# Kernel tuning notes

Hardware: AMD Instinct MI355X
Metric: run time of the kernel (lower is better)

## Reference

```python
import jax, jax.numpy as jnp
import numpy as np

CHUNK = 64

def depthwise_fir(x, filt):
    # x: [B,N,H,D]; filt: [H,D,K]; causal depthwise FIR conv along N
    B, N, H, D = x.shape
    K = filt.shape[-1]
    xc = x.reshape(B, N, H * D).transpose(0, 2, 1)  # [B, HD, N]
    xc = jnp.pad(xc, ((0, 0), (0, 0), (K - 1, 0)))
    w = filt.reshape(H * D, 1, K)
    y = jax.lax.conv_general_dilated(xc, w, (1,), 'VALID',
                                     feature_group_count=H * D,
                                     dimension_numbers=('NCH', 'OIH', 'NCH'))
    return y.transpose(0, 2, 1).reshape(B, N, H, D)

def delta_rule_chunkwise(q, k, v, beta, chunk=CHUNK):
    # DeltaNet chunkwise parallel delta rule. q,k,v:[B,H,L,D], beta:[B,H,L]
    B, H, L, D = q.shape
    q = q * (D ** -0.5)
    k = k / (jnp.linalg.norm(k, axis=-1, keepdims=True) + 1e-6)  # l2-norm keys (DeltaNet convention)
    v = v * beta[..., None]
    k_beta = k * beta[..., None]
    n = L // chunk
    toc = lambda t: t.reshape(B, H, n, chunk, D)
    qc, kc, vc, kbc = toc(q), toc(k), toc(v), toc(k_beta)
    # T = (I + strict_lower(k_beta k^T))^{-1} via triangular solve
    A = jnp.tril(jnp.einsum('bhncd,bhnmd->bhncm', kbc, kc), -1)
    I = jnp.eye(chunk, dtype=q.dtype)
    T = jax.scipy.linalg.solve_triangular(I + A, jnp.broadcast_to(I, A.shape), lower=True)
    u = T @ vc   # [B,H,n,c,D]
    w = T @ kbc  # [B,H,n,c,D]
    def step(S, inp):
        q_i, k_i, u_i, w_i = inp                 # [B,H,c,D]
        u_t = u_i - w_i @ S
        attn_i = jnp.tril(jnp.einsum('bhcd,bhmd->bhcm', q_i, k_i))
        o_i = q_i @ S + attn_i @ u_t
        S = S + jnp.einsum('bhcd,bhce->bhde', k_i, u_t)
        return S, o_i
    xs = tuple(jnp.moveaxis(t, 2, 0) for t in (qc, kc, u, w))
    S0 = jnp.zeros((B, H, D, D), dtype=q.dtype)
    S, o = jax.lax.scan(step, S0, xs)
    o = jnp.moveaxis(o, 0, 2).reshape(B, H, L, D)
    return o, S

def setup_inputs() -> dict:
    key = jax.random.key(0)
    B, N, C, H = 4, 1024, 768, 12
    D = C // H
    P = 5
    ks = jax.random.split(key, 16)
    s = 0.02
    fir_s = jnp.zeros((H, D, 3)).at[..., -1].set(1.0) + 0.01 * jax.random.normal(ks[1], (H, D, 3))
    fir_l = jnp.zeros((H, D, 7)).at[..., -1].set(1.0) + 0.01 * jax.random.normal(ks[2], (H, D, 7))
    return {
        'x': jax.random.normal(ks[0], (B, N, C), jnp.float32),
        'w_qkv': s * jax.random.normal(ks[3], (C, 3 * C)),
        'w_proj': s * jax.random.normal(ks[4], (C, C)),
        'b_proj': jnp.zeros((C,)),
        'fir_short_w': fir_s,
        'fir_long_w': fir_l,
        'mix': 0.02 * jax.random.normal(ks[5], (H, H)),
        'w_prune': s * jax.random.normal(ks[6], (C, H * P)),
        'b_prune': jnp.zeros((H * P,)),
        'w_g1': s * jax.random.normal(ks[7], (C, C)),
        'b_g1': jnp.zeros((C,)),
        'w_g2': s * jax.random.normal(ks[8], (C, H)),
        'b_g2': jnp.zeros((H,)),
        'w_id': s * jax.random.normal(ks[9], (C, C)),
        'id_static_logit': jnp.full((H,), float(np.log(0.2 / 0.8)), jnp.float32),
        'w_idgate': s * jax.random.normal(ks[10], (C, H)),
        'b_idgate': jnp.full((H,), -1.5, jnp.float32),
    }

def reference(x, w_qkv, w_proj, b_proj, fir_short_w, fir_long_w, mix, w_prune,
              b_prune, w_g1, b_g1, w_g2, b_g2, w_id, id_static_logit, w_idgate, b_idgate):
    B, N, C = x.shape
    H = id_static_logit.shape[0]
    D = C // H
    qkv = (x @ w_qkv).reshape(B, N, 3, H, D).transpose(2, 0, 3, 1, 4)  # [3,B,H,N,D]
    q, k, v = qkv[0], qkv[1], qkv[2]
    scale = D ** -0.5
    scores = jnp.einsum('bhqd,bhkd->bhqk', q, k) * scale
    # causal softmax attention (fp8 sage-attention math in full precision)
    neg = jnp.finfo(scores.dtype).min
    causal = jnp.tril(jnp.ones((N, N), dtype=bool))
    attn = jax.nn.softmax(jnp.where(causal, scores, neg), axis=-1)
    attn_out = jnp.einsum('bhqk,bhkd->bnhd'.replace('n', 'q'), attn, v).transpose(0, 2, 1, 3)  # [B,N,H,D] (unused downstream, kept for fidelity)
    v_reshaped = v.transpose(0, 2, 1, 3)  # [B,N,H,D]
    # identity path with static*dynamic gate
    identity_out = (x @ w_id).reshape(B, N, H, D)
    dyn_gate = jax.nn.sigmoid(x @ w_idgate + b_idgate)   # [B,N,H]
    static_gate = jax.nn.sigmoid(id_static_logit)
    identity_out = identity_out * (dyn_gate * static_gate)[..., None]
    # beta = row-sums of (non-causal) softmax, per source (== ~1 numerically)
    beta = jax.nn.softmax(scores, axis=-1).sum(-1)       # [B,H,N]
    delta_out = delta_rule_chunkwise(q, k, v, beta)[0].transpose(0, 2, 1, 3)  # [B,N,H,D]
    # FIR paths + cross-head mixing (residual head-mixing matrix)
    fir_s = depthwise_fir(v_reshaped, fir_short_w)
    fir_l = depthwise_fir(v_reshaped, fir_long_w)
    mix_s = fir_s + jnp.einsum('bnhd,hg->bngd', fir_s, mix)
    mix_l = fir_l + jnp.einsum('bnhd,hg->bngd', fir_l, mix)
    paths = jnp.stack([mix_s, mix_l, delta_out, v_reshaped, identity_out], 0)  # [P,B,N,H,D]
    P = paths.shape[0]
    # progressive pruning: per-head softmax over paths + entropy loss
    wts = jax.nn.softmax((x @ w_prune + b_prune).reshape(B, N, H, P), axis=-1)
    pruned = jnp.einsum('pbnhd,bnhp->bnhd', paths, wts)
    ent1 = -jnp.mean(jnp.sum(wts * jnp.log(wts + 1e-8), -1))
    # context gating: MLP -> per-head sigmoid gate + binary entropy loss
    hdn = jax.nn.gelu(x @ w_g1 + b_g1)
    gate = jax.nn.sigmoid(hdn @ w_g2 + b_g2)             # [B,N,H]
    context = pruned * gate[..., None]
    ent2 = -jnp.mean(gate * jnp.log(gate + 1e-8) + (1 - gate) * jnp.log(1 - gate + 1e-8))
    out = context.reshape(B, N, C) @ w_proj + b_proj
    return out, ent1 + ent2
```

## Files before the change

kernel.cpp:

```cpp
#include <hip/hip_runtime.h>
#include <hip/hip_bf16.h>
#include <math.h>

#define Bz 4
#define Nn 1024
#define Cc 768
#define Hh 12
#define Dd 64
#define BN 4096
#define NC 16
#define BH 48
#define OUT_ELEMS 3145728

#define WS_QKV     0u
#define WS_WSP     9437184u
#define WS_GL      16252928u
#define WS_QS      16777216u
#define WS_KNT     19922944u
#define WS_U       23068672u
#define WS_DELTA   32505856u
#define WS_ENT     38797312u
#define WS_FIRST   38798336u
#define WS_FIRLT   38800640u
#define WS_CBIAS   38806016u
#define WS_GBIAS   38807680u
#define WS_BF16    38807808u
#define SH_XB      0u
#define SH_WQKVT   3145728u
#define SH_WCATT   4915200u
#define SH_G2T     6193152u
#define SH_WPROJT  6291456u
#define SH_HDNB    6881280u
#define SH_CTXB    10027008u

typedef __attribute__((ext_vector_type(8))) short bf16x8;
typedef __attribute__((ext_vector_type(4))) float f32x4;

__device__ __forceinline__ float sigmoidf_(float x) { return 1.f / (1.f + __expf(-x)); }
__device__ __forceinline__ float geluf_(float x) {
    float t = tanhf(0.7978845608028654f * (x + 0.044715f * x * x * x));
    return 0.5f * x * (1.f + t);
}
__device__ __forceinline__ short bf16c(float f) {
    union { float f; unsigned u; } a; a.f = f;
    unsigned r = a.u + 0x7fffu + ((a.u >> 16) & 1u);
    return (short)(r >> 16);
}
__device__ __forceinline__ void gload16(const void* g, void* l) {
    __builtin_amdgcn_global_load_lds(
        (const __attribute__((address_space(1))) unsigned*)g,
        (__attribute__((address_space(3))) unsigned*)l, 16, 0, 0);
}
__device__ __forceinline__ bf16x8 frag_(const short* arr, int row, int kc, int quad) {
    return *(const bf16x8*)&arr[row * 64 + (((kc * 4 + quad) ^ (row & 7)) << 3)];
}

__global__ __launch_bounds__(256) void convert_x_kernel(const float* __restrict__ src,
        short* __restrict__ dst, int n4) {
    int i = blockIdx.x * 256 + threadIdx.x;
    if (i < n4) {
        float4 v = *(const float4*)&src[(size_t)i * 4];
        short4 o;
        o.x = bf16c(v.x); o.y = bf16c(v.y); o.z = bf16c(v.z); o.w = bf16c(v.w);
        *(short4*)&dst[(size_t)i * 4] = o;
    }
}

__global__ __launch_bounds__(256) void convert_w_kernel(const float* __restrict__ w_qkv,
        const float* __restrict__ w_id, const float* __restrict__ w_g1,
        const float* __restrict__ w_proj, short* __restrict__ wqkvT,
        short* __restrict__ wcatT, short* __restrict__ wprojT,
        const float* __restrict__ wp, const float* __restrict__ wig,
        const float* __restrict__ bp, const float* __restrict__ big,
        const float* __restrict__ bg1, const float* __restrict__ bg2,
        const float* __restrict__ wg2, const float* __restrict__ firs,
        const float* __restrict__ firl, short* __restrict__ g2T,
        float* __restrict__ cbias, float* __restrict__ gbias,
        float* __restrict__ firsT, float* __restrict__ firlT) {
    __shared__ float t[64][65];
    const int z = blockIdx.z;
    const int tid = threadIdx.x;
    if (z == 4) {
        int i = (blockIdx.y * 12 + blockIdx.x) * 256 + tid;
        if (i < 98304) {
            int r = i / 768, k = i % 768;
            float wv = 0.f;
            if (r < 60) wv = wp[k * 60 + r];
            else if (r < 72) wv = wig[k * 12 + (r - 60)];
            wcatT[(size_t)(1536 + r) * 768 + k] = (r < 72) ? bf16c(wv) : (short)0;
            g2T[(size_t)r * 768 + k] = (r < 12) ? bf16c(wg2[k * 12 + r]) : (short)0;
        }
        if (i < 1664) {
            float bv = 0.f;
            if (i >= 768 && i < 1536) bv = bg1[i - 768];
            else if (i >= 1536 && i < 1596) bv = bp[i - 1536];
            else if (i >= 1596 && i < 1608) bv = big[i - 1596];
            cbias[i] = bv;
        }
        if (i < 128) gbias[i] = (i < 12) ? bg2[i] : 0.f;
        if (i < 2304) { int tt = i / 768, e = i % 768; firsT[tt * 768 + e] = firs[e * 3 + tt]; }
        if (i < 5376) { int tt = i / 768, e = i % 768; firlT[tt * 768 + e] = firl[e * 7 + tt]; }
        return;
    }
    const float* src; short* dst; int Nw;
    if (z == 0)      { src = w_qkv;  dst = wqkvT;              Nw = 2304; }
    else if (z == 1) { src = w_id;   dst = wcatT;              Nw = 768; }
    else if (z == 2) { src = w_g1;   dst = wcatT + 768 * 768;  Nw = 768; }
    else             { src = w_proj; dst = wprojT;             Nw = 768; }
    const int n0 = blockIdx.y * 64;
    if (n0 >= Nw) return;
    const int k0 = blockIdx.x * 64;
    for (int e = tid; e < 1024; e += 256) {
        int r = e >> 4, c4 = (e & 15) * 4;
        float4 v = *(const float4*)&src[(size_t)(k0 + r) * Nw + n0 + c4];
        t[c4 + 0][r] = v.x; t[c4 + 1][r] = v.y;
        t[c4 + 2][r] = v.z; t[c4 + 3][r] = v.w;
    }
    __syncthreads();
    for (int e = tid; e < 1024; e += 256) {
        int r = e >> 4, c4 = (e & 15) * 4;
        short4 o;
        o.x = bf16c(t[r][c4 + 0]); o.y = bf16c(t[r][c4 + 1]);
        o.z = bf16c(t[r][c4 + 2]); o.w = bf16c(t[r][c4 + 3]);
        *(short4*)&dst[(size_t)(n0 + r) * 768 + k0 + c4] = o;
    }
}

__global__ __launch_bounds__(256) void gemm_mfma(const short* __restrict__ A,
        const short* __restrict__ BT, const float* __restrict__ bias,
        float* __restrict__ C, int M, int N, int K, int glo, int ghi,
        short* __restrict__ C2) {
    __shared__ short As[128 * 64];
    __shared__ short Bs[128 * 64];
    const int tid = threadIdx.x;
    const int lane = tid & 63, w = tid >> 6;
    const int quad = lane >> 4, l15 = lane & 15;
    const int row0 = blockIdx.y * 128, col0 = blockIdx.x * 128;
    const int wm = (w >> 1) * 64, wn = (w & 1) * 64;

    int srow[4]; int scol[4];
#pragma unroll
    for (int i = 0; i < 4; ++i) {
        int G = (w * 4 + i) * 64 + lane;
        int row = G >> 3, g = G & 7;
        srow[i] = row;
        scol[i] = (g ^ (row & 7)) * 8;
    }
    int aoff[4][2], boff[4][2];
#pragma unroll
    for (int mi = 0; mi < 4; ++mi)
#pragma unroll
        for (int kk = 0; kk < 2; ++kk) {
            int ra = wm + mi * 16 + l15;
            aoff[mi][kk] = ra * 128 + (((kk * 4 + quad) ^ (ra & 7)) * 16);
            int rb = wn + mi * 16 + l15;
            boff[mi][kk] = rb * 128 + (((kk * 4 + quad) ^ (rb & 7)) * 16);
        }

    f32x4 acc[4][4];
#pragma unroll
    for (int mi = 0; mi < 4; ++mi)
#pragma unroll
        for (int ni = 0; ni < 4; ++ni) acc[mi][ni] = (f32x4)0.f;

    for (int k0 = 0; k0 < K; k0 += 64) {
#pragma unroll
        for (int i = 0; i < 4; ++i) {
            gload16(&A[(size_t)(row0 + srow[i]) * K + k0 + scol[i]], &As[(w * 4 + i) * 512]);
            gload16(&BT[(size_t)(col0 + srow[i]) * K + k0 + scol[i]], &Bs[(w * 4 + i) * 512]);
        }
        __syncthreads();
#pragma unroll
        for (int kk = 0; kk < 2; ++kk) {
            bf16x8 af[4], bfr[4];
#pragma unroll
            for (int mi = 0; mi < 4; ++mi)
                af[mi] = *(const bf16x8*)((const char*)As + aoff[mi][kk]);
#pragma unroll
            for (int ni = 0; ni < 4; ++ni)
                bfr[ni] = *(const bf16x8*)((const char*)Bs + boff[ni][kk]);
#pragma unroll
            for (int mi = 0; mi < 4; ++mi)
#pragma unroll
                for (int ni = 0; ni < 4; ++ni)
                    acc[mi][ni] = __builtin_amdgcn_mfma_f32_16x16x32_bf16(
                        af[mi], bfr[ni], acc[mi][ni], 0, 0, 0);
        }
        __syncthreads();
    }
#pragma unroll
    for (int ni = 0; ni < 4; ++ni) {
        int col = col0 + wn + ni * 16 + l15;
        float bv = bias ? bias[col] : 0.f;
        bool gel = (col >= glo) && (col < ghi);
#pragma unroll
        for (int mi = 0; mi < 4; ++mi) {
#pragma unroll
            for (int r = 0; r < 4; ++r) {
                int row = row0 + wm + mi * 16 + quad * 4 + r;
                float v = acc[mi][ni][r] + bv;
                if (gel) v = geluf_(v);
                C[(size_t)row * N + col] = v;
                if (C2 && gel) C2[(size_t)row * 768 + (col - glo)] = bf16c(v);
            }
        }
    }
}

__global__ __launch_bounds__(256) void pre_kernel(const float* __restrict__ qkv,
        short* __restrict__ Qsb16, short* __restrict__ Kntb16, float* __restrict__ U,
        short* __restrict__ Wb16, short* __restrict__ Atb16) {
    __shared__ __align__(16) char smem[50176];
    float (*ts)[68] = (float (*)[68])smem;
    short* kn  = (short*)(smem + 17408);
    short* knt = (short*)(smem + 25600);
    short* qsb = (short*)(smem + 33792);
    short* vtb = (short*)(smem + 41984);
    float (*zbuf)[68] = (float (*)[68])(smem + 17408);
    short* tb  = (short*)(smem + 33792);
    const int blk = blockIdx.x;
    const int c = blk & 15, bh = blk >> 4;
    const int b = bh / Hh, h = bh % Hh;
    const int tid = threadIdx.x;
    const int lane = tid & 63, w = tid >> 6;
    const int quad = lane >> 4, l15 = lane & 15;
    const int r = tid >> 2, d0 = (tid & 3) * 16;
    const size_t rowbase = ((size_t)(b * Nn + c * 64)) * (3 * Cc) + h * 64;
    const size_t base2 = (size_t)blk * 4096;

    {
        float4 qq[4], kq[4], vq[4];
        const float* bp_ = &qkv[rowbase + (size_t)r * 2304 + d0];
#pragma unroll
        for (int t4 = 0; t4 < 4; ++t4) qq[t4] = *(const float4*)&bp_[t4 * 4];
#pragma unroll
        for (int t4 = 0; t4 < 4; ++t4) kq[t4] = *(const float4*)&bp_[768 + t4 * 4];
#pragma unroll
        for (int t4 = 0; t4 < 4; ++t4) vq[t4] = *(const float4*)&bp_[1536 + t4 * 4];

        float kf[16];
#pragma unroll
        for (int t4 = 0; t4 < 4; ++t4) {
            kf[t4 * 4 + 0] = kq[t4].x; kf[t4 * 4 + 1] = kq[t4].y;
            kf[t4 * 4 + 2] = kq[t4].z; kf[t4 * 4 + 3] = kq[t4].w;
        }
        float ss = 0.f;
#pragma unroll
        for (int t = 0; t < 16; ++t) ss += kf[t] * kf[t];
        ss += __shfl_xor(ss, 1);
        ss += __shfl_xor(ss, 2);
        float invn = 1.f / (sqrtf(ss) + 1e-6f);
#pragma unroll
        for (int t = 0; t < 16; ++t) kf[t] *= invn;
        {
            bf16x8 g0, g1;
#pragma unroll
            for (int t = 0; t < 8; ++t) { g0[t] = bf16c(kf[t]); g1[t] = bf16c(kf[8 + t]); }
            int gb = d0 >> 3;
            *(bf16x8*)&kn[r * 64 + (((gb + 0) ^ (r & 7)) << 3)] = g0;
            *(bf16x8*)&kn[r * 64 + (((gb + 1) ^ (r & 7)) << 3)] = g1;
#pragma unroll
            for (int t = 0; t < 16; ++t) {
                int d = d0 + t;
                knt[d * 64 + (((r >> 3) ^ (d & 7)) << 3) + (r & 7)] = bf16c(kf[t]);
            }
        }
        {
            float qf[16];
#pragma unroll
            for (int t4 = 0; t4 < 4; ++t4) {
                qf[t4 * 4 + 0] = qq[t4].x * 0.125f; qf[t4 * 4 + 1] = qq[t4].y * 0.125f;
                qf[t4 * 4 + 2] = qq[t4].z * 0.125f; qf[t4 * 4 + 3] = qq[t4].w * 0.125f;
            }
            bf16x8 g0, g1;
#pragma unroll
            for (int t = 0; t < 8; ++t) { g0[t] = bf16c(qf[t]); g1[t] = bf16c(qf[8 + t]); }
            int gb = d0 >> 3;
            *(bf16x8*)&qsb[r * 64 + (((gb + 0) ^ (r & 7)) << 3)] = g0;
            *(bf16x8*)&qsb[r * 64 + (((gb + 1) ^ (r & 7)) << 3)] = g1;
            *(bf16x8*)&Qsb16[base2 + r * 64 + d0] = g0;
            *(bf16x8*)&Qsb16[base2 + r * 64 + d0 + 8] = g1;
        }
#pragma unroll
        for (int t4 = 0; t4 < 4; ++t4) {
            int d = d0 + t4 * 4;
            vtb[(d + 0) * 64 + (((r >> 3) ^ ((d + 0) & 7)) << 3) + (r & 7)] = bf16c(vq[t4].x);
            vtb[(d + 1) * 64 + (((r >> 3) ^ ((d + 1) & 7)) << 3) + (r & 7)] = bf16c(vq[t4].y);
            vtb[(d + 2) * 64 + (((r >> 3) ^ ((d + 2) & 7)) << 3) + (r & 7)] = bf16c(vq[t4].z);
            vtb[(d + 3) * 64 + (((r >> 3) ^ ((d + 3) & 7)) << 3) + (r & 7)] = bf16c(vq[t4].w);
        }
    }
    __syncthreads();

    f32x4 accT[4];
    {
        const int ar = w * 16 + l15;
        bf16x8 aK0 = frag_(kn, ar, 0, quad), aK1 = frag_(kn, ar, 1, quad);
        bf16x8 aQ0 = frag_(qsb, ar, 0, quad), aQ1 = frag_(qsb, ar, 1, quad);
        f32x4 accA[4];
#pragma unroll
        for (int ni = 0; ni < 4; ++ni) {
            int br = ni * 16 + l15;
            bf16x8 b0 = frag_(kn, br, 0, quad), b1 = frag_(kn, br, 1, quad);
            accA[ni] = __builtin_amdgcn_mfma_f32_16x16x32_bf16(aK0, b0, (f32x4)0.f, 0, 0, 0);
            accA[ni] = __builtin_amdgcn_mfma_f32_16x16x32_bf16(aK1, b1, accA[ni], 0, 0, 0);
            accT[ni] = __builtin_amdgcn_mfma_f32_16x16x32_bf16(aQ0, b0, (f32x4)0.f, 0, 0, 0);
            accT[ni] = __builtin_amdgcn_mfma_f32_16x16x32_bf16(aQ1, b1, accT[ni], 0, 0, 0);
        }
#pragma unroll
        for (int ni = 0; ni < 4; ++ni)
#pragma unroll
            for (int reg = 0; reg < 4; ++reg) {
                int row = w * 16 + quad * 4 + reg;
                int col = ni * 16 + l15;
                ts[row][col] = (col < row) ? accA[ni][reg] : 0.f;
            }
    }
    __syncthreads();

    {
        const int R0 = w * 16;
        const int j = lane & 15, s = lane >> 4;
#pragma unroll 1
        for (int i = 0; i < 16; ++i) {
            float p = 0.f;
            for (int m = s; m < i; m += 4)
                p += ts[R0 + i][R0 + m] * ts[R0 + m][R0 + j];
            p += __shfl_xor(p, 16);
            p += __shfl_xor(p, 32);
            if (s == 0) ts[R0 + i][R0 + j] = ((j == i) ? 1.f : 0.f) - p;
        }
    }
    __syncthreads();
#pragma unroll 1
    for (int I = 1; I < 4; ++I) {
        const int ncol = I * 16;
        for (int e = tid; e < 16 * ncol; e += 256) {
            int i = e / ncol, jj = e % ncol;
            float s = 0.f;
            for (int m = jj; m < ncol; ++m) s += ts[ncol + i][m] * ts[m][jj];
            zbuf[i][jj] = s;
        }
        __syncthreads();
        for (int e = tid; e < 16 * ncol; e += 256) {
            int i = e / ncol, jj = e % ncol;
            float s = 0.f;
            for (int ml = 0; ml <= i; ++ml) s += ts[ncol + i][ncol + ml] * zbuf[ml][jj];
            ts[ncol + i][jj] = -s;
        }
        __syncthreads();
    }
    for (int e = tid; e < 512; e += 256) {
        int row = e >> 3, g = e & 7;
        bf16x8 o;
#pragma unroll
        for (int t = 0; t < 8; ++t) o[t] = bf16c(ts[row][g * 8 + t]);
        *(bf16x8*)&tb[row * 64 + ((g ^ (row & 7)) << 3)] = o;
    }
    __syncthreads();

    f32x4 accW[4], accU[4];
    {
        const int ar = w * 16 + l15;
        bf16x8 aT0 = frag_(tb, ar, 0, quad), aT1 = frag_(tb, ar, 1, quad);
#pragma unroll
        for (int ni = 0; ni < 4; ++ni) {
            int br = ni * 16 + l15;
            bf16x8 b0 = frag_(knt, br, 0, quad), b1 = frag_(knt, br, 1, quad);
            bf16x8 c0 = frag_(vtb, br, 0, quad), c1 = frag_(vtb, br, 1, quad);
            accW[ni] = __builtin_amdgcn_mfma_f32_16x16x32_bf16(aT0, b0, (f32x4)0.f, 0, 0, 0);
            accW[ni] = __builtin_amdgcn_mfma_f32_16x16x32_bf16(aT1, b1, accW[ni], 0, 0, 0);
            accU[ni] = __builtin_amdgcn_mfma_f32_16x16x32_bf16(aT0, c0, (f32x4)0.f, 0, 0, 0);
            accU[ni] = __builtin_amdgcn_mfma_f32_16x16x32_bf16(aT1, c1, accU[ni], 0, 0, 0);
        }
    }
#pragma unroll
    for (int ni = 0; ni < 4; ++ni)
#pragma unroll
        for (int reg = 0; reg < 4; ++reg) {
            int row = w * 16 + quad * 4 + reg;
            int col = ni * 16 + l15;
            Wb16[base2 + (size_t)row * 64 + col] = bf16c(accW[ni][reg]);
            U[base2 + (size_t)row * 64 + col] = accU[ni][reg];
            Atb16[base2 + (size_t)row * 64 + col] =
                (col <= row) ? bf16c(accT[ni][reg]) : (short)0;
        }
    for (int e = tid; e < 512; e += 256) {
        int row = e >> 3, gl = e & 7;
        *(bf16x8*)&Kntb16[base2 + row * 64 + ((gl ^ (row & 7)) << 3)] =
            *(const bf16x8*)&knt[row * 64 + (gl << 3)];
    }
}

#define LOADF(cc, F, UU) {                                                     \
    size_t tb_ = ((size_t)(bh * 16 + (cc))) * 4096;                            \
    F##0 = *(const bf16x8*)&Wb16[tb_ + off0];                                  \
    F##1 = *(const bf16x8*)&Wb16[tb_ + off1];                                  \
    F##2 = *(const bf16x8*)&Qsb16[tb_ + off0];                                 \
    F##3 = *(const bf16x8*)&Qsb16[tb_ + off1];                                 \
    F##4 = *(const bf16x8*)&Atb16[tb_ + off0];                                 \
    F##5 = *(const bf16x8*)&Atb16[tb_ + off1];                                 \
    F##6 = *(const bf16x8*)&Kntb16[tb_ + off0];                                \
    F##7 = *(const bf16x8*)&Kntb16[tb_ + off1];                                \
    UU##0 = U[tb_ + urow + 0 * 64]; UU##1 = U[tb_ + urow + 1 * 64];            \
    UU##2 = U[tb_ + urow + 2 * 64]; UU##3 = U[tb_ + urow + 3 * 64]; }

#define BODY(c, F, UU, FN, UN) {                                               \
    int cn_ = ((c) + 1 < 16) ? (c) + 1 : 0;                                    \
    LOADF(cn_, FN, UN);                                                        \
    bf16x8 st0 = *(const bf16x8*)&ST[stoff0];                                  \
    bf16x8 st1 = *(const bf16x8*)&ST[stoff1];                                  \
    bf16x8 nw0, nw1;                                                           \
    _Pragma("unroll") for (int t_ = 0; t_ < 8; ++t_) {                         \
        nw0[t_] = F##0[t_] ^ (short)0x8000;                                    \
        nw1[t_] = F##1[t_] ^ (short)0x8000; }                                  \
    f32x4 ut = {UU##0, UU##1, UU##2, UU##3};                                   \
    ut = __builtin_amdgcn_mfma_f32_16x16x32_bf16(nw0, st0, ut, 0, 0, 0);       \
    ut = __builtin_amdgcn_mfma_f32_16x16x32_bf16(nw1, st1, ut, 0, 0, 0);       \
    f32x4 o = (f32x4)0.f;                                                      \
    o = __builtin_amdgcn_mfma_f32_16x16x32_bf16(F##2, st0, o, 0, 0, 0);        \
    o = __builtin_amdgcn_mfma_f32_16x16x32_bf16(F##3, st1, o, 0, 0, 0);        \
    _Pragma("unroll") for (int j_ = 0; j_ < 4; ++j_) {                         \
        int rr_ = R0 + quad * 4 + j_;                                          \
        UT[l15 * 64 + (((rr_ >> 3) ^ (l15 & 7)) << 3) + (rr_ & 7)] = bf16c(ut[j_]); } \
    __syncthreads();                                                           \
    bf16x8 uf0 = *(const bf16x8*)&UT[stoff0];                                  \
    bf16x8 uf1 = *(const bf16x8*)&UT[stoff1];                                  \
    o = __builtin_amdgcn_mfma_f32_16x16x32_bf16(F##4, uf0, o, 0, 0, 0);        \
    o = __builtin_amdgcn_mfma_f32_16x16x32_bf16(F##5, uf1, o, 0, 0, 0);        \
    S = __builtin_amdgcn_mfma_f32_16x16x32_bf16(F##6, uf0, S, 0, 0, 0);        \
    S = __builtin_amdgcn_mfma_f32_16x16x32_bf16(F##7, uf1, S, 0, 0, 0);        \
    _Pragma("unroll") for (int j_ = 0; j_ < 4; ++j_)                           \
        delta[obase + (size_t)((c) * 64 + j_) * 768] = o[j_];                  \
    _Pragma("unroll") for (int j_ = 0; j_ < 4; ++j_) {                         \
        int dd_ = R0 + quad * 4 + j_;                                          \
        ST[l15 * 64 + (((dd_ >> 3) ^ (l15 & 7)) << 3) + (dd_ & 7)] = bf16c(S[j_]); } \
    __syncthreads(); }

__global__ __launch_bounds__(256) void scan_kernel(const short* __restrict__ Qsb16,
        const short* __restrict__ Kntb16, const float* __restrict__ U,
        const short* __restrict__ Wb16, const short* __restrict__ Atb16,
        float* __restrict__ delta) {
    __shared__ short ST[1024];
    __shared__ short UT[1024];
    const int bh = blockIdx.x;
    const int b = bh / Hh, h = bh % Hh;
    const int g0 = blockIdx.y * 16;
    const int tid = threadIdx.x;
    const int lane = tid & 63, w = tid >> 6;
    const int quad = lane >> 4, l15 = lane & 15;
    const int R0 = w * 16;
    const int off0 = (R0 + l15) * 64 + quad * 8;
    const int off1 = off0 + 32;
    const int urow = (R0 + quad * 4) * 64 + g0 + l15;
    const int stoff0 = l15 * 64 + ((quad ^ (l15 & 7)) << 3);
    const int stoff1 = l15 * 64 + (((4 + quad) ^ (l15 & 7)) << 3);
    const size_t obase = ((size_t)(b * Nn + R0 + quad * 4)) * 768 + h * 64 + g0 + l15;

    for (int e = tid; e < 512; e += 256) ((int*)ST)[e] = 0;
    f32x4 S = (f32x4)0.f;
    bf16x8 fA0, fA1, fA2, fA3, fA4, fA5, fA6, fA7;
    bf16x8 fB0, fB1, fB2, fB3, fB4, fB5, fB6, fB7;
    float uA0, uA1, uA2, uA3, uB0, uB1, uB2, uB3;
    LOADF(0, fA, uA);
    __syncthreads();
#pragma unroll 1
    for (int c = 0; c < 16; c += 2) {
        BODY(c, fA, uA, fB, uB);
        BODY(c + 1, fB, uB, fA, uA);
    }
}

__global__ __launch_bounds__(256) void paths_kernel(const float* __restrict__ qkv,
        const float* __restrict__ delta, const float* __restrict__ wsp,
        const float* __restrict__ gl, const float* __restrict__ mixw,
        const float* __restrict__ idst, const float* __restrict__ firsT,
        const float* __restrict__ firlT, short* __restrict__ ctxb,
        float* __restrict__ entslots) {
    __shared__ float vt[10][768];
    __shared__ float fsb[768], flb[768];
    __shared__ float wts4[4][60], gate4[4][12], idg4[4][12];
    __shared__ float entb[48];
    const int blk = blockIdx.x;
    const int b = blk >> 8, n0 = (blk & 255) * 4;
    const int tid = threadIdx.x;

    for (int t = tid; t < 1920; t += 256) {
        int row = t / 192, c4 = (t % 192) * 4;
        int np = n0 - 6 + row;
        float4 v = make_float4(0.f, 0.f, 0.f, 0.f);
        if (np >= 0) v = *(const float4*)&qkv[((size_t)((b << 10) + np)) * 2304 + 1536 + c4];
        *(float4*)&vt[row][c4] = v;
    }
    if (tid < 48) {
        int ni = tid / 12, h = tid % 12;
        int bn = (b << 10) + n0 + ni;
        const float* pb = &wsp[(size_t)bn * 1664 + 1536];
        float lg[5]; float mx = -1e30f;
#pragma unroll
        for (int p = 0; p < 5; ++p) { lg[p] = pb[h * 5 + p]; mx = fmaxf(mx, lg[p]); }
        float sum = 0.f;
#pragma unroll
        for (int p = 0; p < 5; ++p) { lg[p] = __expf(lg[p] - mx); sum += lg[p]; }
        float e1 = 0.f;
#pragma unroll
        for (int p = 0; p < 5; ++p) {
            float wv = lg[p] / sum;
            wts4[ni][h * 5 + p] = wv;
            e1 += wv * logf(wv + 1e-8f);
        }
        float g = sigmoidf_(gl[(size_t)bn * 128 + h]);
        gate4[ni][h] = g;
        float e2 = g * logf(g + 1e-8f) + (1.f - g) * logf(1.f - g + 1e-8f);
        idg4[ni][h] = sigmoidf_(pb[60 + h]) * sigmoidf_(idst[h]);
        entb[tid] = e1 + e2;
    }
    float4 wl[7], wsv[3];
    if (tid < 192) {
        int c4 = tid * 4;
#pragma unroll
        for (int t = 0; t < 7; ++t) wl[t] = *(const float4*)&firlT[t * 768 + c4];
#pragma unroll
        for (int t = 0; t < 3; ++t) wsv[t] = *(const float4*)&firsT[t * 768 + c4];
    }
    __syncthreads();

#pragma unroll 1
    for (int ni = 0; ni < 4; ++ni) {
        if (tid < 192) {
            int c4 = tid * 4;
            float4 as = make_float4(0.f, 0.f, 0.f, 0.f);
            float4 al = make_float4(0.f, 0.f, 0.f, 0.f);
#pragma unroll
            for (int t = 0; t < 7; ++t) {
                float4 vv = *(const float4*)&vt[ni + t][c4];
                al.x += wl[t].x * vv.x; al.y += wl[t].y * vv.y;
                al.z += wl[t].z * vv.z; al.w += wl[t].w * vv.w;
                if (t >= 4) {
                    as.x += wsv[t - 4].x * vv.x; as.y += wsv[t - 4].y * vv.y;
                    as.z += wsv[t - 4].z * vv.z; as.w += wsv[t - 4].w * vv.w;
                }
            }
            *(float4*)&fsb[c4] = as;
            *(float4*)&flb[c4] = al;
        }
        __syncthreads();
        if (tid < 192) {
            int c4 = tid * 4;
            int h = c4 >> 6, d = c4 & 63;
            float4 ms = *(const float4*)&fsb[c4];
            float4 ml = *(const float4*)&flb[c4];
#pragma unroll
            for (int hh = 0; hh < 12; ++hh) {
                float mw = mixw[hh * 12 + h];
                float4 fsv = *(const float4*)&fsb[hh * 64 + d];
                float4 flv = *(const float4*)&flb[hh * 64 + d];
                ms.x += mw * fsv.x; ms.y += mw * fsv.y;
                ms.z += mw * fsv.z; ms.w += mw * fsv.w;
                ml.x += mw * flv.x; ml.y += mw * flv.y;
                ml.z += mw * flv.z; ml.w += mw * flv.w;
            }
            int bn = (b << 10) + n0 + ni;
            float4 dl = *(const float4*)&delta[(size_t)bn * 768 + c4];
            float4 iv = *(const float4*)&wsp[(size_t)bn * 1664 + c4];
            float4 vv = *(const float4*)&vt[ni + 6][c4];
            float ig = idg4[ni][h];
            const float* wp = &wts4[ni][h * 5];
            float4 pr;
            pr.x = ms.x * wp[0] + ml.x * wp[1] + dl.x * wp[2] + vv.x * wp[3] + iv.x * ig * wp[4];
            pr.y = ms.y * wp[0] + ml.y * wp[1] + dl.y * wp[2] + vv.y * wp[3] + iv.y * ig * wp[4];
            pr.z = ms.z * wp[0] + ml.z * wp[1] + dl.z * wp[2] + vv.z * wp[3] + iv.z * ig * wp[4];
            pr.w = ms.w * wp[0] + ml.w * wp[1] + dl.w * wp[2] + vv.w * wp[3] + iv.w * ig * wp[4];
            float g = gate4[ni][h];
            short4 o;
            o.x = bf16c(pr.x * g); o.y = bf16c(pr.y * g);
            o.z = bf16c(pr.z * g); o.w = bf16c(pr.w * g);
            *(short4*)&ctxb[(size_t)bn * 768 + c4] = o;
        }
        __syncthreads();
    }
    if (tid == 0) {
        float s = 0.f;
#pragma unroll
        for (int i = 0; i < 48; ++i) s += entb[i];
        entslots[blk] = s;
    }
}

__global__ __launch_bounds__(256) void finalize_kernel(const float* __restrict__ slots,
        float* __restrict__ out) {
    __shared__ float red[256];
    const int tid = threadIdx.x;
    float s = 0.f;
    for (int i = tid; i < 1024; i += 256) s += slots[i];
    red[tid] = s;
    __syncthreads();
    for (int off = 128; off > 0; off >>= 1) {
        if (tid < off) red[tid] += red[tid + off];
        __syncthreads();
    }
    if (tid == 0) out[OUT_ELEMS] = -red[0] * (1.f / 49152.f);
}

extern "C" void kernel_launch(void* const* d_in, const int* in_sizes, int n_in,
                              void* d_out, int out_size, void* d_ws, size_t ws_size,
                              hipStream_t stream) {
    const float* x        = (const float*)d_in[0];
    const float* w_qkv    = (const float*)d_in[1];
    const float* w_proj   = (const float*)d_in[2];
    const float* b_proj   = (const float*)d_in[3];
    const float* fir_s_w  = (const float*)d_in[4];
    const float* fir_l_w  = (const float*)d_in[5];
    const float* mixw     = (const float*)d_in[6];
    const float* w_prune  = (const float*)d_in[7];
    const float* b_prune  = (const float*)d_in[8];
    const float* w_g1     = (const float*)d_in[9];
    const float* b_g1     = (const float*)d_in[10];
    const float* w_g2     = (const float*)d_in[11];
    const float* b_g2     = (const float*)d_in[12];
    const float* w_id     = (const float*)d_in[13];
    const float* id_st    = (const float*)d_in[14];
    const float* w_idgate = (const float*)d_in[15];
    const float* b_idgate = (const float*)d_in[16];
    float* out = (float*)d_out;
    float* ws  = (float*)d_ws;

    float* qkv   = ws + WS_QKV;
    float* wsp   = ws + WS_WSP;
    float* gl    = ws + WS_GL;
    short* Qsb16  = (short*)(ws + WS_QS);
    short* Kntb16 = Qsb16 + 3145728;
    short* Wb16   = (short*)(ws + WS_KNT);
    short* Atb16  = Wb16 + 3145728;
    float* Ub    = ws + WS_U;
    float* delta = ws + WS_DELTA;
    float* ent   = ws + WS_ENT;
    float* firsT = ws + WS_FIRST;
    float* firlT = ws + WS_FIRLT;
    float* cbias = ws + WS_CBIAS;
    float* gbias = ws + WS_GBIAS;
    short* wsh   = (short*)(ws + WS_BF16);
    short* xb     = wsh + SH_XB;
    short* wqkvT  = wsh + SH_WQKVT;
    short* wcatT  = wsh + SH_WCATT;
    short* g2T    = wsh + SH_G2T;
    short* wprojT = wsh + SH_WPROJT;
    short* hdnb   = wsh + SH_HDNB;
    short* ctxb   = wsh + SH_CTXB;

    convert_x_kernel<<<dim3(3072), 256, 0, stream>>>(x, xb, 786432);
    convert_w_kernel<<<dim3(12, 36, 5), 256, 0, stream>>>(w_qkv, w_id, w_g1, w_proj,
            wqkvT, wcatT, wprojT, w_prune, w_idgate, b_prune, b_idgate, b_g1, b_g2,
            w_g2, fir_s_w, fir_l_w, g2T, cbias, gbias, firsT, firlT);
    gemm_mfma<<<dim3(18, 32), 256, 0, stream>>>(xb, wqkvT, nullptr, qkv, BN, 2304, 768,
                                                0, 0, nullptr);
    gemm_mfma<<<dim3(13, 32), 256, 0, stream>>>(xb, wcatT, cbias, wsp, BN, 1664, 768,
                                                768, 1536, hdnb);
    gemm_mfma<<<dim3(1, 32), 256, 0, stream>>>(hdnb, g2T, gbias, gl, BN, 128, 768,
                                               0, 0, nullptr);
    pre_kernel<<<dim3(BH * NC), 256, 0, stream>>>(qkv, Qsb16, Kntb16, Ub, Wb16, Atb16);
    scan_kernel<<<dim3(BH, 4), 256, 0, stream>>>(Qsb16, Kntb16, Ub, Wb16, Atb16, delta);
    paths_kernel<<<dim3(1024), 256, 0, stream>>>(qkv, delta, wsp, gl, mixw, id_st,
                                                 firsT, firlT, ctxb, ent);
    gemm_mfma<<<dim3(6, 32), 256, 0, stream>>>(ctxb, wprojT, b_proj, out, BN, 768, 768,
                                               0, 0, nullptr);
    finalize_kernel<<<1, 256, 0, stream>>>(ent, out);
}
```

Measured before the change: 286.2 us.

## Merge QKV and side-projection GEMMs and store intermediates in bf16

The separate QKV GEMM and the identity/gate/prune GEMM become one wide GEMM over a concatenated weight matrix, which scatters its bf16 outputs to per-purpose buffers in the epilogue. The qkv, identity-output and delta intermediates move from fp32 to bf16, so downstream pre, scan and paths kernels read and write half the bytes. The intent is to cut a launch, reuse the A tile across all outputs and reduce memory traffic. In exchange, more intermediates are rounded to bf16, which adds precision loss, especially in the delta-rule inputs.

```diff
diff --git a/kernel.cpp b/kernel.cpp
--- a/kernel.cpp
+++ b/kernel.cpp
@@ -12,26 +12,28 @@
 #define BH 48
 #define OUT_ELEMS 3145728
 
-#define WS_QKV     0u
-#define WS_WSP     9437184u
-#define WS_GL      16252928u
-#define WS_QS      16777216u
-#define WS_KNT     19922944u
-#define WS_U       23068672u
-#define WS_DELTA   32505856u
-#define WS_ENT     38797312u
-#define WS_FIRST   38798336u
-#define WS_FIRLT   38800640u
-#define WS_CBIAS   38806016u
-#define WS_GBIAS   38807680u
-#define WS_BF16    38807808u
+#define WS_U       0u
+#define WS_PLIG    3145728u
+#define WS_GL      3670016u
+#define WS_ENT     4194304u
+#define WS_FIRST   4195328u
+#define WS_FIRLT   4197632u
+#define WS_CBIAS   4203008u
+#define WS_GBIAS   4206976u
+#define WS_SH      4207104u
 #define SH_XB      0u
-#define SH_WQKVT   3145728u
-#define SH_WCATT   4915200u
-#define SH_G2T     6193152u
-#define SH_WPROJT  6291456u
-#define SH_HDNB    6881280u
-#define SH_CTXB    10027008u
+#define SH_QKVB    3145728u
+#define SH_IDOUT   12582912u
+#define SH_HDNB    15728640u
+#define SH_CTXB    18874368u
+#define SH_DELTA   22020096u
+#define SH_QS      25165824u
+#define SH_KNT     28311552u
+#define SH_W       31457280u
+#define SH_AT      34603008u
+#define SH_WCAT2T  37748736u
+#define SH_G2T     40796160u
+#define SH_WPROJT  40894464u
 
 typedef __attribute__((ext_vector_type(8))) short bf16x8;
 typedef __attribute__((ext_vector_type(4))) float f32x4;
@@ -45,6 +47,11 @@
     union { float f; unsigned u; } a; a.f = f;
     unsigned r = a.u + 0x7fffu + ((a.u >> 16) & 1u);
     return (short)(r >> 16);
+}
+__device__ __forceinline__ float b2f(short s) {
+    union { float f; unsigned u; } a;
+    a.u = ((unsigned)(unsigned short)s) << 16;
+    return a.f;
 }
 __device__ __forceinline__ void gload16(const void* g, void* l) {
     __builtin_amdgcn_global_load_lds(
@@ -68,8 +75,8 @@
 
 __global__ __launch_bounds__(256) void convert_w_kernel(const float* __restrict__ w_qkv,
         const float* __restrict__ w_id, const float* __restrict__ w_g1,
-        const float* __restrict__ w_proj, short* __restrict__ wqkvT,
-        short* __restrict__ wcatT, short* __restrict__ wprojT,
+        const float* __restrict__ w_proj, short* __restrict__ wcat2T,
+        short* __restrict__ wprojT,
         const float* __restrict__ wp, const float* __restrict__ wig,
         const float* __restrict__ bp, const float* __restrict__ big,
         const float* __restrict__ bg1, const float* __restrict__ bg2,
@@ -87,14 +94,14 @@
             float wv = 0.f;
             if (r < 60) wv = wp[k * 60 + r];
             else if (r < 72) wv = wig[k * 12 + (r - 60)];
-            wcatT[(size_t)(1536 + r) * 768 + k] = (r < 72) ? bf16c(wv) : (short)0;
+            wcat2T[(size_t)(3840 + r) * 768 + k] = (r < 72) ? bf16c(wv) : (short)0;
             g2T[(size_t)r * 768 + k] = (r < 12) ? bf16c(wg2[k * 12 + r]) : (short)0;
         }
-        if (i < 1664) {
+        if (i < 3968) {
             float bv = 0.f;
-            if (i >= 768 && i < 1536) bv = bg1[i - 768];
-            else if (i >= 1536 && i < 1596) bv = bp[i - 1536];
-            else if (i >= 1596 && i < 1608) bv = big[i - 1596];
+            if (i >= 3072 && i < 3840) bv = bg1[i - 3072];
+            else if (i >= 3840 && i < 3900) bv = bp[i - 3840];
+            else if (i >= 3900 && i < 3912) bv = big[i - 3900];
             cbias[i] = bv;
         }
         if (i < 128) gbias[i] = (i < 12) ? bg2[i] : 0.f;
@@ -103,10 +110,10 @@
         return;
     }
     const float* src; short* dst; int Nw;
-    if (z == 0)      { src = w_qkv;  dst = wqkvT;              Nw = 2304; }
-    else if (z == 1) { src = w_id;   dst = wcatT;              Nw = 768; }
-    else if (z == 2) { src = w_g1;   dst = wcatT + 768 * 768;  Nw = 768; }
-    else             { src = w_proj; dst = wprojT;             Nw = 768; }
+    if (z == 0)      { src = w_qkv;  dst = wcat2T;               Nw = 2304; }
+    else if (z == 1) { src = w_id;   dst = wcat2T + 2304 * 768;  Nw = 768; }
+    else if (z == 2) { src = w_g1;   dst = wcat2T + 3072 * 768;  Nw = 768; }
+    else             { src = w_proj; dst = wprojT;               Nw = 768; }
     const int n0 = blockIdx.y * 64;
     if (n0 >= Nw) return;
     const int k0 = blockIdx.x * 64;
@@ -126,88 +133,103 @@
     }
 }
 
+#define GEMM_CORE(APTR, BPTR, KDIM)                                            \
+    __shared__ short As[128 * 64];                                             \
+    __shared__ short Bs[128 * 64];                                             \
+    const int tid = threadIdx.x;                                               \
+    const int lane = tid & 63, w = tid >> 6;                                   \
+    const int quad = lane >> 4, l15 = lane & 15;                               \
+    const int row0 = blockIdx.y * 128, col0 = blockIdx.x * 128;                \
+    const int wm = (w >> 1) * 64, wn = (w & 1) * 64;                           \
+    int srow[4]; int scol[4];                                                  \
+    _Pragma("unroll") for (int i = 0; i < 4; ++i) {                            \
+        int G = (w * 4 + i) * 64 + lane;                                       \
+        int row = G >> 3, g = G & 7;                                           \
+        srow[i] = row;                                                         \
+        scol[i] = (g ^ (row & 7)) * 8;                                         \
+    }                                                                          \
+    int aoff[4][2], boff[4][2];                                                \
+    _Pragma("unroll") for (int mi = 0; mi < 4; ++mi)                           \
+        _Pragma("unroll") for (int kk = 0; kk < 2; ++kk) {                     \
+            int ra = wm + mi * 16 + l15;                                       \
+            aoff[mi][kk] = ra * 128 + (((kk * 4 + quad) ^ (ra & 7)) * 16);     \
+            int rb = wn + mi * 16 + l15;                                       \
+            boff[mi][kk] = rb * 128 + (((kk * 4 + quad) ^ (rb & 7)) * 16);     \
+        }                                                                      \
+    f32x4 acc[4][4];                                                           \
+    _Pragma("unroll") for (int mi = 0; mi < 4; ++mi)                           \
+        _Pragma("unroll") for (int ni = 0; ni < 4; ++ni) acc[mi][ni] = (f32x4)0.f; \
+    for (int k0 = 0; k0 < (KDIM); k0 += 64) {                                  \
+        _Pragma("unroll") for (int i = 0; i < 4; ++i) {                        \
+            gload16(&(APTR)[(size_t)(row0 + srow[i]) * (KDIM) + k0 + scol[i]], \
+                    &As[(w * 4 + i) * 512]);                                   \
+            gload16(&(BPTR)[(size_t)(col0 + srow[i]) * (KDIM) + k0 + scol[i]], \
+                    &Bs[(w * 4 + i) * 512]);                                   \
+        }                                                                      \
+        __syncthreads();                                                       \
+        _Pragma("unroll") for (int kk = 0; kk < 2; ++kk) {                     \
+            bf16x8 af[4], bfr[4];                                              \
+            _Pragma("unroll") for (int mi = 0; mi < 4; ++mi)                   \
+                af[mi] = *(const bf16x8*)((const char*)As + aoff[mi][kk]);     \
+            _Pragma("unroll") for (int ni = 0; ni < 4; ++ni)                   \
+                bfr[ni] = *(const bf16x8*)((const char*)Bs + boff[ni][kk]);    \
+            _Pragma("unroll") for (int mi = 0; mi < 4; ++mi)                   \
+                _Pragma("unroll") for (int ni = 0; ni < 4; ++ni)               \
+                    acc[mi][ni] = __builtin_amdgcn_mfma_f32_16x16x32_bf16(     \
+                        af[mi], bfr[ni], acc[mi][ni], 0, 0, 0);                \
+        }                                                                      \
+        __syncthreads();                                                       \
+    }
+
+__global__ __launch_bounds__(256) void gemm_main(const short* __restrict__ A,
+        const short* __restrict__ BT, const float* __restrict__ bias,
+        short* __restrict__ qkvb, short* __restrict__ idoutb,
+        short* __restrict__ hdnb, float* __restrict__ plig) {
+    GEMM_CORE(A, BT, 768)
+#pragma unroll
+    for (int ni = 0; ni < 4; ++ni) {
+        int col = col0 + wn + ni * 16 + l15;
+        float bv = bias[col];
+#pragma unroll
+        for (int mi = 0; mi < 4; ++mi) {
+#pragma unroll
+            for (int r = 0; r < 4; ++r) {
+                int row = row0 + wm + mi * 16 + quad * 4 + r;
+                float v = acc[mi][ni][r] + bv;
+                if (col < 2304) {
+                    qkvb[(size_t)row * 2304 + col] = bf16c(v);
+                } else if (col < 3072) {
+                    idoutb[(size_t)row * 768 + (col - 2304)] = bf16c(v);
+                } else if (col < 3840) {
+                    hdnb[(size_t)row * 768 + (col - 3072)] = bf16c(geluf_(v));
+                } else {
+                    plig[(size_t)row * 128 + (col - 3840)] = v;
+                }
+            }
+        }
+    }
+}
+
 __global__ __launch_bounds__(256) void gemm_mfma(const short* __restrict__ A,
         const short* __restrict__ BT, const float* __restrict__ bias,
-        float* __restrict__ C, int M, int N, int K, int glo, int ghi,
-        short* __restrict__ C2) {
-    __shared__ short As[128 * 64];
-    __shared__ short Bs[128 * 64];
-    const int tid = threadIdx.x;
-    const int lane = tid & 63, w = tid >> 6;
-    const int quad = lane >> 4, l15 = lane & 15;
-    const int row0 = blockIdx.y * 128, col0 = blockIdx.x * 128;
-    const int wm = (w >> 1) * 64, wn = (w & 1) * 64;
-
-    int srow[4]; int scol[4];
-#pragma unroll
-    for (int i = 0; i < 4; ++i) {
-        int G = (w * 4 + i) * 64 + lane;
-        int row = G >> 3, g = G & 7;
-        srow[i] = row;
-        scol[i] = (g ^ (row & 7)) * 8;
-    }
-    int aoff[4][2], boff[4][2];
-#pragma unroll
-    for (int mi = 0; mi < 4; ++mi)
-#pragma unroll
-        for (int kk = 0; kk < 2; ++kk) {
-            int ra = wm + mi * 16 + l15;
-            aoff[mi][kk] = ra * 128 + (((kk * 4 + quad) ^ (ra & 7)) * 16);
-            int rb = wn + mi * 16 + l15;
-            boff[mi][kk] = rb * 128 + (((kk * 4 + quad) ^ (rb & 7)) * 16);
-        }
-
-    f32x4 acc[4][4];
-#pragma unroll
-    for (int mi = 0; mi < 4; ++mi)
-#pragma unroll
-        for (int ni = 0; ni < 4; ++ni) acc[mi][ni] = (f32x4)0.f;
-
-    for (int k0 = 0; k0 < K; k0 += 64) {
-#pragma unroll
-        for (int i = 0; i < 4; ++i) {
-            gload16(&A[(size_t)(row0 + srow[i]) * K + k0 + scol[i]], &As[(w * 4 + i) * 512]);
-            gload16(&BT[(size_t)(col0 + srow[i]) * K + k0 + scol[i]], &Bs[(w * 4 + i) * 512]);
-        }
-        __syncthreads();
-#pragma unroll
-        for (int kk = 0; kk < 2; ++kk) {
-            bf16x8 af[4], bfr[4];
-#pragma unroll
-            for (int mi = 0; mi < 4; ++mi)
-                af[mi] = *(const bf16x8*)((const char*)As + aoff[mi][kk]);
-#pragma unroll
-            for (int ni = 0; ni < 4; ++ni)
-                bfr[ni] = *(const bf16x8*)((const char*)Bs + boff[ni][kk]);
-#pragma unroll
-            for (int mi = 0; mi < 4; ++mi)
-#pragma unroll
-                for (int ni = 0; ni < 4; ++ni)
-                    acc[mi][ni] = __builtin_amdgcn_mfma_f32_16x16x32_bf16(
-                        af[mi], bfr[ni], acc[mi][ni], 0, 0, 0);
-        }
-        __syncthreads();
-    }
+        float* __restrict__ C, int M, int N, int K) {
+    GEMM_CORE(A, BT, K)
 #pragma unroll
     for (int ni = 0; ni < 4; ++ni) {
         int col = col0 + wn + ni * 16 + l15;
         float bv = bias ? bias[col] : 0.f;
-        bool gel = (col >= glo) && (col < ghi);
 #pragma unroll
         for (int mi = 0; mi < 4; ++mi) {
 #pragma unroll
             for (int r = 0; r < 4; ++r) {
                 int row = row0 + wm + mi * 16 + quad * 4 + r;
-                float v = acc[mi][ni][r] + bv;
-                if (gel) v = geluf_(v);
-                C[(size_t)row * N + col] = v;
-                if (C2 && gel) C2[(size_t)row * 768 + (col - glo)] = bf16c(v);
-            }
-        }
-    }
-}
-
-__global__ __launch_bounds__(256) void pre_kernel(const float* __restrict__ qkv,
+                C[(size_t)row * N + col] = acc[mi][ni][r] + bv;
+            }
+        }
+    }
+}
+
+__global__ __launch_bounds__(256) void pre_kernel(const short* __restrict__ qkvb,
         short* __restrict__ Qsb16, short* __restrict__ Kntb16, float* __restrict__ U,
         short* __restrict__ Wb16, short* __restrict__ Atb16) {
     __shared__ __align__(16) char smem[50176];
@@ -225,56 +247,48 @@
     const int lane = tid & 63, w = tid >> 6;
     const int quad = lane >> 4, l15 = lane & 15;
     const int r = tid >> 2, d0 = (tid & 3) * 16;
-    const size_t rowbase = ((size_t)(b * Nn + c * 64)) * (3 * Cc) + h * 64;
+    const size_t rowb = ((size_t)(b * Nn + c * 64)) * 2304 + h * 64;
     const size_t base2 = (size_t)blk * 4096;
 
     {
-        float4 qq[4], kq[4], vq[4];
-        const float* bp_ = &qkv[rowbase + (size_t)r * 2304 + d0];
-#pragma unroll
-        for (int t4 = 0; t4 < 4; ++t4) qq[t4] = *(const float4*)&bp_[t4 * 4];
-#pragma unroll
-        for (int t4 = 0; t4 < 4; ++t4) kq[t4] = *(const float4*)&bp_[768 + t4 * 4];
-#pragma unroll
-        for (int t4 = 0; t4 < 4; ++t4) vq[t4] = *(const float4*)&bp_[1536 + t4 * 4];
+        const short* qp = &qkvb[rowb + (size_t)r * 2304 + d0];
+        bf16x8 qb0 = *(const bf16x8*)&qp[0],    qb1 = *(const bf16x8*)&qp[8];
+        bf16x8 kb0 = *(const bf16x8*)&qp[768],  kb1 = *(const bf16x8*)&qp[776];
+        bf16x8 vb0 = *(const bf16x8*)&qp[1536], vb1 = *(const bf16x8*)&qp[1544];
 
         float kf[16];
 #pragma unroll
-        for (int t4 = 0; t4 < 4; ++t4) {
-            kf[t4 * 4 + 0] = kq[t4].x; kf[t4 * 4 + 1] = kq[t4].y;
-            kf[t4 * 4 + 2] = kq[t4].z; kf[t4 * 4 + 3] = kq[t4].w;
-        }
+        for (int t = 0; t < 8; ++t) { kf[t] = b2f(kb0[t]); kf[8 + t] = b2f(kb1[t]); }
         float ss = 0.f;
 #pragma unroll
         for (int t = 0; t < 16; ++t) ss += kf[t] * kf[t];
         ss += __shfl_xor(ss, 1);
         ss += __shfl_xor(ss, 2);
         float invn = 1.f / (sqrtf(ss) + 1e-6f);
-#pragma unroll
-        for (int t = 0; t < 16; ++t) kf[t] *= invn;
         {
             bf16x8 g0, g1;
 #pragma unroll
-            for (int t = 0; t < 8; ++t) { g0[t] = bf16c(kf[t]); g1[t] = bf16c(kf[8 + t]); }
+            for (int t = 0; t < 8; ++t) {
+                g0[t] = bf16c(kf[t] * invn); g1[t] = bf16c(kf[8 + t] * invn);
+            }
             int gb = d0 >> 3;
             *(bf16x8*)&kn[r * 64 + (((gb + 0) ^ (r & 7)) << 3)] = g0;
             *(bf16x8*)&kn[r * 64 + (((gb + 1) ^ (r & 7)) << 3)] = g1;
 #pragma unroll
-            for (int t = 0; t < 16; ++t) {
+            for (int t = 0; t < 8; ++t) {
                 int d = d0 + t;
-                knt[d * 64 + (((r >> 3) ^ (d & 7)) << 3) + (r & 7)] = bf16c(kf[t]);
+                knt[d * 64 + (((r >> 3) ^ (d & 7)) << 3) + (r & 7)] = g0[t];
+                int d2 = d0 + 8 + t;
+                knt[d2 * 64 + (((r >> 3) ^ (d2 & 7)) << 3) + (r & 7)] = g1[t];
             }
         }
         {
-            float qf[16];
-#pragma unroll
-            for (int t4 = 0; t4 < 4; ++t4) {
-                qf[t4 * 4 + 0] = qq[t4].x * 0.125f; qf[t4 * 4 + 1] = qq[t4].y * 0.125f;
-                qf[t4 * 4 + 2] = qq[t4].z * 0.125f; qf[t4 * 4 + 3] = qq[t4].w * 0.125f;
-            }
             bf16x8 g0, g1;
 #pragma unroll
-            for (int t = 0; t < 8; ++t) { g0[t] = bf16c(qf[t]); g1[t] = bf16c(qf[8 + t]); }
+            for (int t = 0; t < 8; ++t) {
+                g0[t] = bf16c(b2f(qb0[t]) * 0.125f);
+                g1[t] = bf16c(b2f(qb1[t]) * 0.125f);
+            }
             int gb = d0 >> 3;
             *(bf16x8*)&qsb[r * 64 + (((gb + 0) ^ (r & 7)) << 3)] = g0;
             *(bf16x8*)&qsb[r * 64 + (((gb + 1) ^ (r & 7)) << 3)] = g1;
@@ -282,12 +296,11 @@
             *(bf16x8*)&Qsb16[base2 + r * 64 + d0 + 8] = g1;
         }
 #pragma unroll
-        for (int t4 = 0; t4 < 4; ++t4) {
-            int d = d0 + t4 * 4;
-            vtb[(d + 0) * 64 + (((r >> 3) ^ ((d + 0) & 7)) << 3) + (r & 7)] = bf16c(vq[t4].x);
-            vtb[(d + 1) * 64 + (((r >> 3) ^ ((d + 1) & 7)) << 3) + (r & 7)] = bf16c(vq[t4].y);
-            vtb[(d + 2) * 64 + (((r >> 3) ^ ((d + 2) & 7)) << 3) + (r & 7)] = bf16c(vq[t4].z);
-            vtb[(d + 3) * 64 + (((r >> 3) ^ ((d + 3) & 7)) << 3) + (r & 7)] = bf16c(vq[t4].w);
+        for (int t = 0; t < 8; ++t) {
+            int d = d0 + t;
+            vtb[d * 64 + (((r >> 3) ^ (d & 7)) << 3) + (r & 7)] = vb0[t];
+            int d2 = d0 + 8 + t;
+            vtb[d2 * 64 + (((r >> 3) ^ (d2 & 7)) << 3) + (r & 7)] = vb1[t];
         }
     }
     __syncthreads();
@@ -431,7 +444,7 @@
     S = __builtin_amdgcn_mfma_f32_16x16x32_bf16(F##6, uf0, S, 0, 0, 0);        \
     S = __builtin_amdgcn_mfma_f32_16x16x32_bf16(F##7, uf1, S, 0, 0, 0);        \
     _Pragma("unroll") for (int j_ = 0; j_ < 4; ++j_)                           \
-        delta[obase + (size_t)((c) * 64 + j_) * 768] = o[j_];                  \
+        deltab[obase + (size_t)((c) * 64 + j_) * 768] = bf16c(o[j_]);          \
     _Pragma("unroll") for (int j_ = 0; j_ < 4; ++j_) {                         \
         int dd_ = R0 + quad * 4 + j_;                                          \
         ST[l15 * 64 + (((dd_ >> 3) ^ (l15 & 7)) << 3) + (dd_ & 7)] = bf16c(S[j_]); } \
@@ -440,7 +453,7 @@
 __global__ __launch_bounds__(256) void scan_kernel(const short* __restrict__ Qsb16,
         const short* __restrict__ Kntb16, const float* __restrict__ U,
         const short* __restrict__ Wb16, const short* __restrict__ Atb16,
-        float* __restrict__ delta) {
+        short* __restrict__ deltab) {
     __shared__ short ST[1024];
     __shared__ short UT[1024];
     const int bh = blockIdx.x;
@@ -471,12 +484,12 @@
     }
 }
 
-__global__ __launch_bounds__(256) void paths_kernel(const float* __restrict__ qkv,
-        const float* __restrict__ delta, const float* __restrict__ wsp,
-        const float* __restrict__ gl, const float* __restrict__ mixw,
-        const float* __restrict__ idst, const float* __restrict__ firsT,
-        const float* __restrict__ firlT, short* __restrict__ ctxb,
-        float* __restrict__ entslots) {
+__global__ __launch_bounds__(256) void paths_kernel(const short* __restrict__ qkvb,
+        const short* __restrict__ deltab, const short* __restrict__ idoutb,
+        const float* __restrict__ plig, const float* __restrict__ gl,
+        const float* __restrict__ mixw, const float* __restrict__ idst,
+        const float* __restrict__ firsT, const float* __restrict__ firlT,
+        short* __restrict__ ctxb, float* __restrict__ entslots) {
     __shared__ float vt[10][768];
     __shared__ float fsb[768], flb[768];
     __shared__ float wts4[4][60], gate4[4][12], idg4[4][12];
@@ -485,17 +498,23 @@
     const int b = blk >> 8, n0 = (blk & 255) * 4;
     const int tid = threadIdx.x;
 
-    for (int t = tid; t < 1920; t += 256) {
-        int row = t / 192, c4 = (t % 192) * 4;
+    for (int t = tid; t < 960; t += 256) {
+        int row = t / 96, c8 = (t % 96) * 8;
         int np = n0 - 6 + row;
-        float4 v = make_float4(0.f, 0.f, 0.f, 0.f);
-        if (np >= 0) v = *(const float4*)&qkv[((size_t)((b << 10) + np)) * 2304 + 1536 + c4];
-        *(float4*)&vt[row][c4] = v;
+        float4 lo = make_float4(0.f, 0.f, 0.f, 0.f);
+        float4 hi = make_float4(0.f, 0.f, 0.f, 0.f);
+        if (np >= 0) {
+            bf16x8 vv = *(const bf16x8*)&qkvb[((size_t)((b << 10) + np)) * 2304 + 1536 + c8];
+            lo.x = b2f(vv[0]); lo.y = b2f(vv[1]); lo.z = b2f(vv[2]); lo.w = b2f(vv[3]);
+            hi.x = b2f(vv[4]); hi.y = b2f(vv[5]); hi.z = b2f(vv[6]); hi.w = b2f(vv[7]);
+        }
+        *(float4*)&vt[row][c8] = lo;
+        *(float4*)&vt[row][c8 + 4] = hi;
     }
     if (tid < 48) {
         int ni = tid / 12, h = tid % 12;
         int bn = (b << 10) + n0 + ni;
-        const float* pb = &wsp[(size_t)bn * 1664 + 1536];
+        const float* pb = &plig[(size_t)bn * 128];
         float lg[5]; float mx = -1e30f;
 #pragma unroll
         for (int p = 0; p < 5; ++p) { lg[p] = pb[h * 5 + p]; mx = fmaxf(mx, lg[p]); }
@@ -561,16 +580,16 @@
                 ml.z += mw * flv.z; ml.w += mw * flv.w;
             }
             int bn = (b << 10) + n0 + ni;
-            float4 dl = *(const float4*)&delta[(size_t)bn * 768 + c4];
-            float4 iv = *(const float4*)&wsp[(size_t)bn * 1664 + c4];
+            short4 ds = *(const short4*)&deltab[(size_t)bn * 768 + c4];
+            short4 is = *(const short4*)&idoutb[(size_t)bn * 768 + c4];
             float4 vv = *(const float4*)&vt[ni + 6][c4];
             float ig = idg4[ni][h];
             const float* wp = &wts4[ni][h * 5];
             float4 pr;
-            pr.x = ms.x * wp[0] + ml.x * wp[1] + dl.x * wp[2] + vv.x * wp[3] + iv.x * ig * wp[4];
-            pr.y = ms.y * wp[0] + ml.y * wp[1] + dl.y * wp[2] + vv.y * wp[3] + iv.y * ig * wp[4];
-            pr.z = ms.z * wp[0] + ml.z * wp[1] + dl.z * wp[2] + vv.z * wp[3] + iv.z * ig * wp[4];
-            pr.w = ms.w * wp[0] + ml.w * wp[1] + dl.w * wp[2] + vv.w * wp[3] + iv.w * ig * wp[4];
+            pr.x = ms.x * wp[0] + ml.x * wp[1] + b2f(ds.x) * wp[2] + vv.x * wp[3] + b2f(is.x) * ig * wp[4];
+            pr.y = ms.y * wp[0] + ml.y * wp[1] + b2f(ds.y) * wp[2] + vv.y * wp[3] + b2f(is.y) * ig * wp[4];
+            pr.z = ms.z * wp[0] + ml.z * wp[1] + b2f(ds.z) * wp[2] + vv.z * wp[3] + b2f(is.z) * ig * wp[4];
+            pr.w = ms.w * wp[0] + ml.w * wp[1] + b2f(ds.w) * wp[2] + vv.w * wp[3] + b2f(is.w) * ig * wp[4];
             float g = gate4[ni][h];
             short4 o;
             o.x = bf16c(pr.x * g); o.y = bf16c(pr.y * g);
@@ -625,44 +644,40 @@
     float* out = (float*)d_out;
     float* ws  = (float*)d_ws;
 
-    float* qkv   = ws + WS_QKV;
-    float* wsp   = ws + WS_WSP;
+    float* Ub    = ws + WS_U;
+    float* plig  = ws + WS_PLIG;
     float* gl    = ws + WS_GL;
-    short* Qsb16  = (short*)(ws + WS_QS);
-    short* Kntb16 = Qsb16 + 3145728;
-    short* Wb16   = (short*)(ws + WS_KNT);
-    short* Atb16  = Wb16 + 3145728;
-    float* Ub    = ws + WS_U;
-    float* delta = ws + WS_DELTA;
     float* ent   = ws + WS_ENT;
     float* firsT = ws + WS_FIRST;
     float* firlT = ws + WS_FIRLT;
     float* cbias = ws + WS_CBIAS;
     float* gbias = ws + WS_GBIAS;
-    short* wsh   = (short*)(ws + WS_BF16);
-    short* xb     = wsh + SH_XB;
-    short* wqkvT  = wsh + SH_WQKVT;
-    short* wcatT  = wsh + SH_WCATT;
-    short* g2T    = wsh + SH_G2T;
-    short* wprojT = wsh + SH_WPROJT;
-    short* hdnb   = wsh + SH_HDNB;
-    short* ctxb   = wsh + SH_CTXB;
+    short* wsh   = (short*)(ws + WS_SH);
+    short* xb      = wsh + SH_XB;
+    short* qkvb    = wsh + SH_QKVB;
+    short* idoutb  = wsh + SH_IDOUT;
+    short* hdnb    = wsh + SH_HDNB;
+    short* ctxb    = wsh + SH_CTXB;
+    short* deltab  = wsh + SH_DELTA;
+    short* Qsb16   = wsh + SH_QS;
+    short* Kntb16  = wsh + SH_KNT;
+    short* Wb16    = wsh + SH_W;
+    short* Atb16   = wsh + SH_AT;
+    short* wcat2T  = wsh + SH_WCAT2T;
+    short* g2T     = wsh + SH_G2T;
+    short* wprojT  = wsh + SH_WPROJT;
 
     convert_x_kernel<<<dim3(3072), 256, 0, stream>>>(x, xb, 786432);
     convert_w_kernel<<<dim3(12, 36, 5), 256, 0, stream>>>(w_qkv, w_id, w_g1, w_proj,
-            wqkvT, wcatT, wprojT, w_prune, w_idgate, b_prune, b_idgate, b_g1, b_g2,
+            wcat2T, wprojT, w_prune, w_idgate, b_prune, b_idgate, b_g1, b_g2,
             w_g2, fir_s_w, fir_l_w, g2T, cbias, gbias, firsT, firlT);
-    gemm_mfma<<<dim3(18, 32), 256, 0, stream>>>(xb, wqkvT, nullptr, qkv, BN, 2304, 768,
-                                                0, 0, nullptr);
-    gemm_mfma<<<dim3(13, 32), 256, 0, stream>>>(xb, wcatT, cbias, wsp, BN, 1664, 768,
-                                                768, 1536, hdnb);
-    gemm_mfma<<<dim3(1, 32), 256, 0, stream>>>(hdnb, g2T, gbias, gl, BN, 128, 768,
-                                               0, 0, nullptr);
-    pre_kernel<<<dim3(BH * NC), 256, 0, stream>>>(qkv, Qsb16, Kntb16, Ub, Wb16, Atb16);
-    scan_kernel<<<dim3(BH, 4), 256, 0, stream>>>(Qsb16, Kntb16, Ub, Wb16, Atb16, delta);
-    paths_kernel<<<dim3(1024), 256, 0, stream>>>(qkv, delta, wsp, gl, mixw, id_st,
-                                                 firsT, firlT, ctxb, ent);
-    gemm_mfma<<<dim3(6, 32), 256, 0, stream>>>(ctxb, wprojT, b_proj, out, BN, 768, 768,
-                                               0, 0, nullptr);
+    gemm_main<<<dim3(31, 32), 256, 0, stream>>>(xb, wcat2T, cbias,
+                                                qkvb, idoutb, hdnb, plig);
+    gemm_mfma<<<dim3(1, 32), 256, 0, stream>>>(hdnb, g2T, gbias, gl, BN, 128, 768);
+    pre_kernel<<<dim3(BH * NC), 256, 0, stream>>>(qkvb, Qsb16, Kntb16, Ub, Wb16, Atb16);
+    scan_kernel<<<dim3(BH, 4), 256, 0, stream>>>(Qsb16, Kntb16, Ub, Wb16, Atb16, deltab);
+    paths_kernel<<<dim3(1024), 256, 0, stream>>>(qkvb, deltab, idoutb, plig, gl,
+                                                 mixw, id_st, firsT, firlT, ctxb, ent);
+    gemm_mfma<<<dim3(6, 32), 256, 0, stream>>>(ctxb, wprojT, b_proj, out, BN, 768, 768);
     finalize_kernel<<<1, 256, 0, stream>>>(ent, out);
 }
```

Measured after the change: 273.5 us. 1.05x faster.
